# Optimization experiments

Measured on AMD Instinct MI355X. Metric: run time of the kernel, lower is better.

## Reference

```python
import jax, jax.numpy as jnp
import numpy as np

K1, K2 = 0.01, 0.03
DATA_RANGE = 1.0
EPS = 1e-6


def setup_inputs() -> dict:
    key = jax.random.key(0)
    k1, k2, k3 = jax.random.split(key, 3)
    B, C, H, W = 4, 3, 256, 176
    S, M = 5, 18
    X = jax.random.normal(k1, (B, C, H, W), dtype=jnp.float32)
    Y = jax.random.normal(k2, (B, C, H, W), dtype=jnp.float32)
    bp_mask = jax.random.uniform(k3, (B, S, M, H, W), dtype=jnp.float32)
    return {"X": X, "Y": Y, "bp_mask": bp_mask}


def reference(X, Y, bp_mask):
    # Rescale from [-1, 1] to [0, 1]
    X = (X + 1.0) / 2.0
    Y = (Y + 1.0) / 2.0
    C1 = (K1 * DATA_RANGE) ** 2
    C2 = (K2 * DATA_RANGE) ** 2

    # Normalized mask weights: [B, S, M, H, W]
    msum = bp_mask.sum(axis=(-2, -1), keepdims=True)
    w = bp_mask / (msum + EPS)

    # Masked first / second moments -> [B, S, M, C], no repeated 6D tensors
    mu1 = jnp.einsum('bchw,bsmhw->bsmc', X, w)
    mu2 = jnp.einsum('bchw,bsmhw->bsmc', Y, w)
    mu11 = jnp.einsum('bchw,bsmhw->bsmc', X * X, w)
    mu22 = jnp.einsum('bchw,bsmhw->bsmc', Y * Y, w)
    mu12 = jnp.einsum('bchw,bsmhw->bsmc', X * Y, w)

    mu1_sq = mu1 * mu1
    mu2_sq = mu2 * mu2
    mu1_mu2 = mu1 * mu2
    sigma1_sq = mu11 - mu1_sq
    sigma2_sq = mu22 - mu2_sq
    sigma12 = mu12 - mu1_mu2

    cs = (2.0 * sigma12 + C2) / (sigma1_sq + sigma2_sq + C2)
    ssim = (2.0 * mu1_mu2 + C1) / (mu1_sq + mu2_sq + C1) * cs
    # nonnegative_ssim=True
    ssim = jax.nn.relu(ssim)
    cs = jax.nn.relu(cs)

    # Mean over merged (M, C) axis -> [B, S]
    cs_batch = cs.mean(axis=(2, 3))
    ssim_batch = ssim.mean(axis=(2, 3))

    msssim = jnp.prod(cs_batch[:, :-1], axis=1) * ssim_batch[:, -1]
    return msssim.mean()
```

## Files before the change

kernel.cpp:

```cpp
#include <hip/hip_runtime.h>

#define B_  4
#define C_  3
#define S_  5
#define M_  18
#define HW  45056
#define HW4 (HW/4)
#define SPLIT 4
#define TPB 256
#define CHUNK4 (HW4/SPLIT)
#define ITERS (CHUNK4/TPB)
#define NPLANE (B_*S_*M_)
#define NBLK (NPLANE*SPLIT)


__global__ __launch_bounds__(TPB) void moments_kernel(
    const float4* __restrict__ X, const float4* __restrict__ Y,
    const float4* __restrict__ Mk, float* __restrict__ part) {
  int wg    = (blockIdx.x & 7) * (NBLK / 8) + (blockIdx.x >> 3);
  int plane = wg / SPLIT;
  int chunk = wg - plane * SPLIT;
  int b     = plane / (S_ * M_);

  const float4* mp = Mk + (size_t)plane * HW4;
  const float4* xp = X  + (size_t)b * (C_ * HW4);
  const float4* yp = Y  + (size_t)b * (C_ * HW4);

  int base = chunk * CHUNK4 + (int)threadIdx.x;

  float aW = 0.f;
  float a1[C_], a2[C_], a11[C_], a22[C_], a12[C_];
#pragma unroll
  for (int c = 0; c < C_; ++c) { a1[c]=a2[c]=a11[c]=a22[c]=a12[c]=0.f; }

#pragma unroll
  for (int it = 0; it < ITERS; ++it) {
    int i = base + it * TPB;
    float4 w  = mp[i];
    aW += (w.x + w.y) + (w.z + w.w);
    float wf[4] = {w.x, w.y, w.z, w.w};
#pragma unroll
    for (int c = 0; c < C_; ++c) {
      float4 xv = xp[c * HW4 + i];
      float4 yv = yp[c * HW4 + i];
      float xf[4] = {xv.x, xv.y, xv.z, xv.w};
      float yf[4] = {yv.x, yv.y, yv.z, yv.w};
#pragma unroll
      for (int j = 0; j < 4; ++j) {
        float xc = xf[j], yc = yf[j], wc = wf[j];
        float wx = wc * xc;
        float wy = wc * yc;
        a1 [c] += wx;
        a2 [c] += wy;
        a11[c]  = fmaf(wx, xc, a11[c]);
        a22[c]  = fmaf(wy, yc, a22[c]);
        a12[c]  = fmaf(wx, yc, a12[c]);
      }
    }
  }

  float v[16];
  v[0] = aW;
#pragma unroll
  for (int c = 0; c < C_; ++c) {
    v[1 + c*5 + 0] = a1[c];
    v[1 + c*5 + 1] = a2[c];
    v[1 + c*5 + 2] = a11[c];
    v[1 + c*5 + 3] = a22[c];
    v[1 + c*5 + 4] = a12[c];
  }

#pragma unroll
  for (int off = 32; off > 0; off >>= 1) {
#pragma unroll
    for (int j = 0; j < 16; ++j) v[j] += __shfl_xor(v[j], off);
  }

  __shared__ float red[TPB/64][16];
  int lane = threadIdx.x & 63;
  int wv   = threadIdx.x >> 6;
  if (lane == 0) {
#pragma unroll
    for (int j = 0; j < 16; ++j) red[wv][j] = v[j];
  }
  __syncthreads();
  if (threadIdx.x < 16) {
    float s = (red[0][threadIdx.x] + red[1][threadIdx.x]) +
              (red[2][threadIdx.x] + red[3][threadIdx.x]);
    part[(size_t)wg * 16 + threadIdx.x] = s;
  }
}

__global__ __launch_bounds__(384) void finalize_kernel(
    const float* __restrict__ part, float* __restrict__ out) {
  __shared__ float csS[NPLANE], ssS[NPLANE];
  __shared__ double csb[B_*S_], ssb[B_*S_];
  int t = threadIdx.x;

  if (t < NPLANE) {
    double s[16];
#pragma unroll
    for (int j = 0; j < 16; ++j) s[j] = 0.0;
    for (int ch = 0; ch < SPLIT; ++ch) {
      const float* p = part + (size_t)(t * SPLIT + ch) * 16;
#pragma unroll
      for (int j = 0; j < 16; ++j) s[j] += (double)p[j];
    }
    const double C1d = 1e-4, C2d = 9e-4;
    double W = s[0];
    double inv = 1.0 / (W + 1e-6);
    double csAcc = 0.0, ssAcc = 0.0;
#pragma unroll
    for (int c = 0; c < C_; ++c) {
      double S1  = s[1 + c*5 + 0];
      double S2  = s[1 + c*5 + 1];
      double S11 = s[1 + c*5 + 2];
      double S22 = s[1 + c*5 + 3];
      double S12 = s[1 + c*5 + 4];
      double mu1  = (0.5*S1 + 0.5*W) * inv;
      double mu2  = (0.5*S2 + 0.5*W) * inv;
      double mu11 = (0.25*S11 + 0.5*S1 + 0.25*W) * inv;
      double mu22 = (0.25*S22 + 0.5*S2 + 0.25*W) * inv;
      double mu12 = (0.25*(S12 + S1 + S2 + W)) * inv;
      double m1s = mu1*mu1, m2s = mu2*mu2, m12 = mu1*mu2;
      double sig1  = mu11 - m1s;
      double sig2  = mu22 - m2s;
      double sig12 = mu12 - m12;
      double cs   = (2.0*sig12 + C2d) / (sig1 + sig2 + C2d);
      double ssim = (2.0*m12 + C1d) / (m1s + m2s + C1d) * cs;
      if (cs   < 0.0) cs   = 0.0;
      if (ssim < 0.0) ssim = 0.0;
      csAcc += cs; ssAcc += ssim;
    }
    csS[t] = (float)csAcc;
    ssS[t] = (float)ssAcc;
  }
  __syncthreads();

  if (t < B_*S_) {
    double cb = 0.0, sb = 0.0;
    for (int m = 0; m < M_; ++m) { cb += (double)csS[t*M_ + m]; sb += (double)ssS[t*M_ + m]; }
    csb[t] = cb / (double)(M_*C_);
    ssb[t] = sb / (double)(M_*C_);
  }
  __syncthreads();

  if (t == 0) {
    double acc = 0.0;
    for (int b = 0; b < B_; ++b) {
      double p = ssb[b*S_ + (S_-1)];
      for (int s = 0; s < S_-1; ++s) p *= csb[b*S_ + s];
      acc += p;
    }
    out[0] = (float)(acc / (double)B_);
  }
}

extern "C" void kernel_launch(void* const* d_in, const int* in_sizes, int n_in,
                              void* d_out, int out_size, void* d_ws, size_t ws_size,
                              hipStream_t stream) {
  (void)in_sizes; (void)n_in; (void)out_size; (void)ws_size;
  const float4* X  = (const float4*)d_in[0];
  const float4* Y  = (const float4*)d_in[1];
  const float4* Mk = (const float4*)d_in[2];
  float* part = (float*)d_ws;
  float* out  = (float*)d_out;

  hipLaunchKernelGGL(moments_kernel, dim3(NBLK), dim3(TPB), 0, stream,
                     X, Y, Mk, part);
  hipLaunchKernelGGL(finalize_kernel, dim3(1), dim3(384), 0, stream, part, out);
}
```

Baseline: 121.7 us.

## Group three mask planes per 768-thread block to share X/Y loads

Each block now handles three mask planes of the same (b,s) using three 256-thread groups. A __syncthreads at the top of each iteration keeps the groups in lockstep so their identical X/Y loads hit cache together. The aim is to cut redundant X/Y fetches from L2/HBM. In exchange it adds a barrier every iteration, uses larger blocks and launches fewer of them, and each thread still issues its own X/Y loads.

```diff
diff --git a/kernel.cpp b/kernel.cpp
--- a/kernel.cpp
+++ b/kernel.cpp
@@ -7,26 +7,35 @@
 #define HW  45056
 #define HW4 (HW/4)
 #define SPLIT 4
-#define TPB 256
+#define TPB 768
+#define GTPB 256
+#define G   3
+#define MG  (M_/G)
 #define CHUNK4 (HW4/SPLIT)
-#define ITERS (CHUNK4/TPB)
+#define ITERS (CHUNK4/GTPB)
+#define NGROUP (B_*S_*MG)
+#define NBLK (NGROUP*SPLIT)
 #define NPLANE (B_*S_*M_)
-#define NBLK (NPLANE*SPLIT)
-
 
 __global__ __launch_bounds__(TPB) void moments_kernel(
     const float4* __restrict__ X, const float4* __restrict__ Y,
     const float4* __restrict__ Mk, float* __restrict__ part) {
   int wg    = (blockIdx.x & 7) * (NBLK / 8) + (blockIdx.x >> 3);
-  int plane = wg / SPLIT;
-  int chunk = wg - plane * SPLIT;
-  int b     = plane / (S_ * M_);
+  int pg    = wg / SPLIT;
+  int chunk = wg - pg * SPLIT;
+  int bs    = pg / MG;
+  int mg    = pg - bs * MG;
+  int b     = bs / S_;
 
+  int grp  = threadIdx.x >> 8;
+  int gtid = threadIdx.x & 255;
+
+  int plane = bs * M_ + mg * G + grp;
   const float4* mp = Mk + (size_t)plane * HW4;
   const float4* xp = X  + (size_t)b * (C_ * HW4);
   const float4* yp = Y  + (size_t)b * (C_ * HW4);
 
-  int base = chunk * CHUNK4 + (int)threadIdx.x;
+  int base = chunk * CHUNK4 + gtid;
 
   float aW = 0.f;
   float a1[C_], a2[C_], a11[C_], a22[C_], a12[C_];
@@ -35,8 +44,9 @@
 
 #pragma unroll
   for (int it = 0; it < ITERS; ++it) {
-    int i = base + it * TPB;
-    float4 w  = mp[i];
+    __syncthreads();
+    int i = base + it * GTPB;
+    float4 w = mp[i];
     aW += (w.x + w.y) + (w.z + w.w);
     float wf[4] = {w.x, w.y, w.z, w.w};
 #pragma unroll
@@ -84,10 +94,11 @@
     for (int j = 0; j < 16; ++j) red[wv][j] = v[j];
   }
   __syncthreads();
-  if (threadIdx.x < 16) {
-    float s = (red[0][threadIdx.x] + red[1][threadIdx.x]) +
-              (red[2][threadIdx.x] + red[3][threadIdx.x]);
-    part[(size_t)wg * 16 + threadIdx.x] = s;
+  if (gtid < 16) {
+    int w0 = grp * 4;
+    float s = (red[w0+0][gtid] + red[w0+1][gtid]) +
+              (red[w0+2][gtid] + red[w0+3][gtid]);
+    part[(size_t)(plane * SPLIT + chunk) * 16 + gtid] = s;
   }
 }
 
```

After: 124.1 us. About the same (+1.9%).

## Split moments kernel work across channels to triple block count

Applied to the files above, without the earlier changes.

Each block now handles a single channel of one mask plane chunk instead of all three channels, so the grid grows by a factor of C and each thread carries 6 accumulators instead of 16. The aim is more parallelism and lower register pressure, which should give better occupancy and more memory requests in flight. In exchange the mask plane (the largest input) is read three times, once per channel block, which relies on L2/MALL cache reuse to avoid roughly tripling mask traffic. The finalize kernel is updated for the new partial layout.

```diff
diff --git a/kernel.cpp b/kernel.cpp
--- a/kernel.cpp
+++ b/kernel.cpp
@@ -11,83 +11,71 @@
 #define CHUNK4 (HW4/SPLIT)
 #define ITERS (CHUNK4/TPB)
 #define NPLANE (B_*S_*M_)
-#define NBLK (NPLANE*SPLIT)
+#define NBLK (NPLANE*C_*SPLIT)
+#define NV 6
 
 
 __global__ __launch_bounds__(TPB) void moments_kernel(
     const float4* __restrict__ X, const float4* __restrict__ Y,
     const float4* __restrict__ Mk, float* __restrict__ part) {
-  int wg    = (blockIdx.x & 7) * (NBLK / 8) + (blockIdx.x >> 3);
-  int plane = wg / SPLIT;
-  int chunk = wg - plane * SPLIT;
-  int b     = plane / (S_ * M_);
+  int wg     = (blockIdx.x & 7) * (NBLK / 8) + (blockIdx.x >> 3);
+  int pc     = wg / SPLIT;
+  int chunk  = wg - pc * SPLIT;
+  int plane  = pc / C_;
+  int c      = pc - plane * C_;
+  int b      = plane / (S_ * M_);
 
   const float4* mp = Mk + (size_t)plane * HW4;
-  const float4* xp = X  + (size_t)b * (C_ * HW4);
-  const float4* yp = Y  + (size_t)b * (C_ * HW4);
+  const float4* xp = X  + (size_t)(b * C_ + c) * HW4;
+  const float4* yp = Y  + (size_t)(b * C_ + c) * HW4;
 
   int base = chunk * CHUNK4 + (int)threadIdx.x;
 
-  float aW = 0.f;
-  float a1[C_], a2[C_], a11[C_], a22[C_], a12[C_];
-#pragma unroll
-  for (int c = 0; c < C_; ++c) { a1[c]=a2[c]=a11[c]=a22[c]=a12[c]=0.f; }
+  float aW = 0.f, s1 = 0.f, s2 = 0.f, s11 = 0.f, s22 = 0.f, s12 = 0.f;
 
 #pragma unroll
   for (int it = 0; it < ITERS; ++it) {
     int i = base + it * TPB;
     float4 w  = mp[i];
-    aW += (w.x + w.y) + (w.z + w.w);
-    float wf[4] = {w.x, w.y, w.z, w.w};
+    float4 xv = xp[i];
+    float4 yv = yp[i];
+    float wf[4] = {w.x,  w.y,  w.z,  w.w};
+    float xf[4] = {xv.x, xv.y, xv.z, xv.w};
+    float yf[4] = {yv.x, yv.y, yv.z, yv.w};
 #pragma unroll
-    for (int c = 0; c < C_; ++c) {
-      float4 xv = xp[c * HW4 + i];
-      float4 yv = yp[c * HW4 + i];
-      float xf[4] = {xv.x, xv.y, xv.z, xv.w};
-      float yf[4] = {yv.x, yv.y, yv.z, yv.w};
-#pragma unroll
-      for (int j = 0; j < 4; ++j) {
-        float xc = xf[j], yc = yf[j], wc = wf[j];
-        float wx = wc * xc;
-        float wy = wc * yc;
-        a1 [c] += wx;
-        a2 [c] += wy;
-        a11[c]  = fmaf(wx, xc, a11[c]);
-        a22[c]  = fmaf(wy, yc, a22[c]);
-        a12[c]  = fmaf(wx, yc, a12[c]);
-      }
+    for (int j = 0; j < 4; ++j) {
+      float xc = xf[j], yc = yf[j], wc = wf[j];
+      float wx = wc * xc;
+      float wy = wc * yc;
+      aW  += wc;
+      s1  += wx;
+      s2  += wy;
+      s11  = fmaf(wx, xc, s11);
+      s22  = fmaf(wy, yc, s22);
+      s12  = fmaf(wx, yc, s12);
     }
   }
 
-  float v[16];
-  v[0] = aW;
-#pragma unroll
-  for (int c = 0; c < C_; ++c) {
-    v[1 + c*5 + 0] = a1[c];
-    v[1 + c*5 + 1] = a2[c];
-    v[1 + c*5 + 2] = a11[c];
-    v[1 + c*5 + 3] = a22[c];
-    v[1 + c*5 + 4] = a12[c];
-  }
+  float v[NV] = {aW, s1, s2, s11, s22, s12};
 
 #pragma unroll
   for (int off = 32; off > 0; off >>= 1) {
 #pragma unroll
-    for (int j = 0; j < 16; ++j) v[j] += __shfl_xor(v[j], off);
+    for (int j = 0; j < NV; ++j) v[j] += __shfl_xor(v[j], off);
   }
 
-  __shared__ float red[TPB/64][16];
+  __shared__ float red[TPB/64][NV];
   int lane = threadIdx.x & 63;
   int wv   = threadIdx.x >> 6;
   if (lane == 0) {
 #pragma unroll
-    for (int j = 0; j < 16; ++j) red[wv][j] = v[j];
+    for (int j = 0; j < NV; ++j) red[wv][j] = v[j];
   }
   __syncthreads();
-  if (threadIdx.x < 16) {
+  if (threadIdx.x < NV) {
     float s = (red[0][threadIdx.x] + red[1][threadIdx.x]) +
               (red[2][threadIdx.x] + red[3][threadIdx.x]);
-    part[(size_t)wg * 16 + threadIdx.x] = s;
+    part[(size_t)wg * NV + threadIdx.x] = s;
   }
 }
 
@@ -98,25 +86,24 @@
   int t = threadIdx.x;
 
   if (t < NPLANE) {
-    double s[16];
-#pragma unroll
-    for (int j = 0; j < 16; ++j) s[j] = 0.0;
-    for (int ch = 0; ch < SPLIT; ++ch) {
-      const float* p = part + (size_t)(t * SPLIT + ch) * 16;
-#pragma unroll
-      for (int j = 0; j < 16; ++j) s[j] += (double)p[j];
-    }
+    double W = 0.0;
+    for (int ch = 0; ch < SPLIT; ++ch)
+      W += (double)part[(size_t)((t * C_ + 0) * SPLIT + ch) * NV + 0];
+
     const double C1d = 1e-4, C2d = 9e-4;
-    double W = s[0];
     double inv = 1.0 / (W + 1e-6);
     double csAcc = 0.0, ssAcc = 0.0;
 #pragma unroll
     for (int c = 0; c < C_; ++c) {
-      double S1  = s[1 + c*5 + 0];
-      double S2  = s[1 + c*5 + 1];
-      double S11 = s[1 + c*5 + 2];
-      double S22 = s[1 + c*5 + 3];
-      double S12 = s[1 + c*5 + 4];
+      double S1 = 0.0, S2 = 0.0, S11 = 0.0, S22 = 0.0, S12 = 0.0;
+      for (int ch = 0; ch < SPLIT; ++ch) {
+        const float* p = part + (size_t)((t * C_ + c) * SPLIT + ch) * NV;
+        S1  += (double)p[1];
+        S2  += (double)p[2];
+        S11 += (double)p[3];
+        S22 += (double)p[4];
+        S12 += (double)p[5];
+      }
       double mu1  = (0.5*S1 + 0.5*W) * inv;
       double mu2  = (0.5*S2 + 0.5*W) * inv;
       double mu11 = (0.25*S11 + 0.5*S1 + 0.25*W) * inv;
```

After: 126.1 us. 1.04x slower.
